# Performance work log

Measured on AMD Instinct MI355X. Metric: run time of the kernel, lower is better.

Reference implementation:

```python
import jax, jax.numpy as jnp
import numpy as np

NEG = -1.0e9
LN_EPS = 1e-5

B, S, M = 16, 1024, 256
H, L = 8, 2
DK = M // H  # 32


def setup_inputs() -> dict:
    key = jax.random.key(0)
    ks = jax.random.split(key, 10)
    adj = jax.random.randint(ks[0], (B, S, S), 0, 2).astype(jnp.int32)
    inputs = jax.random.normal(ks[1], (B, S, M), dtype=jnp.float32)
    score_mask = jax.random.randint(ks[2], (B, 1, S, S), 0, 2).astype(bool)
    # learned params: per layer H head projections Linear(M, DK), one attn Linear(2*DK, 1), LayerNorm(M)
    sc = 1.0 / np.sqrt(M)
    proj_w = jax.random.uniform(ks[3], (L, H, M, DK), jnp.float32, -sc, sc)
    proj_b = jax.random.uniform(ks[4], (L, H, DK), jnp.float32, -sc, sc)
    sa = 1.0 / np.sqrt(2 * DK)
    attn_w = jax.random.uniform(ks[5], (L, 2 * DK), jnp.float32, -sa, sa)
    attn_b = jax.random.uniform(ks[6], (L,), jnp.float32, -sa, sa)
    ln_g = jnp.ones((L, M), jnp.float32)
    ln_b = jnp.zeros((L, M), jnp.float32)
    return {"adj": adj, "inputs": inputs, "score_mask": score_mask, "type": 0,
            "proj_w": proj_w, "proj_b": proj_b, "attn_w": attn_w, "attn_b": attn_b,
            "ln_g": ln_g, "ln_b": ln_b}


def _layer(x, adj_l, smask, pw, pb, aw, ab, g, b):
    # x: [B,S,M]; per-head projection -> [B,H,S,DK]
    P = jnp.einsum('bsm,hmd->bhsd', x, pw) + pb[None, :, None, :]
    a1, a2 = aw[:DK], aw[DK:]
    # additive attention decomposed: score[b,h,i,j] = leaky_relu(a1.P_i + a2.P_j + ab)
    s1 = jnp.einsum('bhsd,d->bhs', P, a1)
    s2 = jnp.einsum('bhsd,d->bhs', P, a2)
    score = s1[..., :, None] + s2[..., None, :] + ab
    score = jnp.where(score >= 0, score, 0.2 * score)  # leaky_relu(0.2)
    score = jnp.where(smask, NEG, score)               # score_mask[:,0] broadcast over heads
    if adj_l is not None:
        score = jnp.where(adj_l[:, None] == 0, NEG, score)
    attn = jax.nn.softmax(score, axis=-1)
    out = jnp.einsum('bhij,bhjd->bhid', attn, P)       # [B,H,S,DK]
    concat = out.transpose(0, 2, 1, 3).reshape(x.shape[0], x.shape[1], -1)
    r = x + concat
    mu = jnp.mean(r, axis=-1, keepdims=True)
    var = jnp.mean((r - mu) ** 2, axis=-1, keepdims=True)
    return (r - mu) * jax.lax.rsqrt(var + LN_EPS) * g + b


def reference(adj, inputs, score_mask, type, proj_w, proj_b, attn_w, attn_b, ln_g, ln_b):
    # eval mode: DropBlock and both dropouts are identity
    semantic = (type == 1)
    smask = score_mask[:, 0][:, None]  # [B,1,S,S]
    x = inputs
    for l in range(L):
        adj_l = None if (semantic and l > 0) else adj
        x = _layer(x, adj_l, smask, proj_w[l], proj_b[l], attn_w[l], attn_b[l], ln_g[l], ln_b[l])
    return x
```

## Files before the change

### kernel.cpp

```cpp
#include <hip/hip_runtime.h>
#include <hip/hip_bf16.h>
#include <hip/hip_fp16.h>
#include <math.h>

#define NB 16
#define NS 1024
#define NM 256
#define NH 8
#define NDK 32
#define NL 2

typedef __attribute__((ext_vector_type(4))) float f32x4;
typedef __attribute__((ext_vector_type(8))) short bf16x8;
typedef __attribute__((ext_vector_type(4))) short bf16x4u;
typedef __attribute__((ext_vector_type(8))) _Float16 f16x8;
typedef __attribute__((ext_vector_type(2))) _Float16 f16x2;

#if __has_builtin(__builtin_amdgcn_exp2f)
#define EXP2F(x) __builtin_amdgcn_exp2f(x)
#else
#define EXP2F(x) exp2f(x)
#endif

__device__ __forceinline__ unsigned short f2h(float f) {
  _Float16 h = (_Float16)f;
  return __builtin_bit_cast(unsigned short, h);
}
__device__ __forceinline__ float h2f(unsigned short u) {
  return (float)__builtin_bit_cast(_Float16, u);
}

__device__ __forceinline__ unsigned int wword(unsigned int pw, unsigned int nw,
                                              f16x2 e1p2, f16x2 e1n2,
                                              unsigned int mk) {
  f16x2 hp = __builtin_bit_cast(f16x2, pw);
  f16x2 hn = __builtin_bit_cast(f16x2, nw);
  f16x2 w = __builtin_elementwise_max(hp * e1p2, hn * e1n2);
  return __builtin_bit_cast(unsigned int, w) & mk;
}

__global__ __launch_bounds__(256) void packbits_kernel(
    const int* __restrict__ src, unsigned int* __restrict__ dst, int inv)
{
  int wid = blockIdx.x * 4 + (threadIdx.x >> 6);
  int lane = threadIdx.x & 63;
  size_t eb = (size_t)wid * 2048;
  const int4* a4 = (const int4*)(src + eb);
  int lg = lane >> 3;
  int sh = (lane & 7) * 4;
  unsigned int xo = inv ? 15u : 0u;
#pragma unroll
  for (int k = 0; k < 8; ++k) {
    int4 v = a4[k * 64 + lane];
    unsigned int nc = ((v.x != 0) ? 1u : 0u) | ((v.y != 0) ? 2u : 0u) |
                      ((v.z != 0) ? 4u : 0u) | ((v.w != 0) ? 8u : 0u);
    nc ^= xo;
    unsigned int vc = nc << sh;
    vc |= __shfl_xor(vc, 1, 64);
    vc |= __shfl_xor(vc, 2, 64);
    vc |= __shfl_xor(vc, 4, 64);
    if ((lane & 7) == 0) dst[(size_t)wid * 64 + k * 8 + lg] = vc;
  }
}

__global__ __launch_bounds__(256) void maskcomb_kernel(
    unsigned int* __restrict__ pkc, const unsigned int* __restrict__ pks)
{
  int t = blockIdx.x * 256 + threadIdx.x;
  uint4 a = ((uint4*)pkc)[t];
  uint4 s = ((const uint4*)pks)[t];
  a.x |= s.x; a.y |= s.y; a.z |= s.z; a.w |= s.w;
  ((uint4*)pkc)[t] = a;
}

__global__ __launch_bounds__(256) void proj_kernel(
    const float* __restrict__ x,
    const float* __restrict__ pw,
    const float* __restrict__ pb,
    unsigned short* __restrict__ Pt)
{
  __shared__ unsigned short As[64][40];
  __shared__ unsigned short Bs[64][40];

  int ct = blockIdx.x;
  int rt = blockIdx.y;
  int t = threadIdx.x;
  int w = t >> 6, lane = t & 63;
  int il = lane & 15, g4 = lane >> 4;
  int wi = w >> 1, wc = w & 1;

  f32x4 acc[2][2] = {};

  int arow = t >> 2, akoff = (t & 3) * 8;
  int bcol = t & 63, bk0 = (t >> 6) * 8;
  int hd = ct * 64 + bcol;
  int h = hd >> 5, d = hd & 31;

  for (int k0 = 0; k0 < NM; k0 += 32) {
    const float* xp = x + (size_t)(rt * 64 + arow) * NM + k0 + akoff;
    f32x4 v0 = *(const f32x4*)xp;
    f32x4 v1 = *(const f32x4*)(xp + 4);
    unsigned short av[8];
    av[0] = f2h(v0[0]); av[1] = f2h(v0[1]); av[2] = f2h(v0[2]); av[3] = f2h(v0[3]);
    av[4] = f2h(v1[0]); av[5] = f2h(v1[1]); av[6] = f2h(v1[2]); av[7] = f2h(v1[3]);
    *(bf16x8*)&As[arow][akoff] = *(bf16x8*)av;
    const float* wp = pw + (size_t)h * NM * NDK + (size_t)(k0 + bk0) * NDK + d;
    unsigned short bv[8];
#pragma unroll
    for (int q = 0; q < 8; ++q) bv[q] = f2h(wp[q * NDK]);
    *(bf16x8*)&Bs[bcol][bk0] = *(bf16x8*)bv;
    __syncthreads();

    f16x8 af0 = *(f16x8*)&As[wi * 32 + il][g4 * 8];
    f16x8 af1 = *(f16x8*)&As[wi * 32 + 16 + il][g4 * 8];
    f16x8 bf0 = *(f16x8*)&Bs[wc * 32 + il][g4 * 8];
    f16x8 bf1 = *(f16x8*)&Bs[wc * 32 + 16 + il][g4 * 8];
    acc[0][0] = __builtin_amdgcn_mfma_f32_16x16x32_f16(af0, bf0, acc[0][0], 0, 0, 0);
    acc[0][1] = __builtin_amdgcn_mfma_f32_16x16x32_f16(af0, bf1, acc[0][1], 0, 0, 0);
    acc[1][0] = __builtin_amdgcn_mfma_f32_16x16x32_f16(af1, bf0, acc[1][0], 0, 0, 0);
    acc[1][1] = __builtin_amdgcn_mfma_f32_16x16x32_f16(af1, bf1, acc[1][1], 0, 0, 0);
    __syncthreads();
  }

#pragma unroll
  for (int ih = 0; ih < 2; ++ih) {
#pragma unroll
    for (int dh = 0; dh < 2; ++dh) {
      int colhd = ct * 64 + wc * 32 + dh * 16 + il;
      int hh = colhd >> 5, dd = colhd & 31;
      float bias = pb[colhd];
      int r0 = rt * 64 + wi * 32 + ih * 16 + g4 * 4;
      int bb = r0 >> 10, ss = r0 & 1023;
      f32x4 c = acc[ih][dh];
      unsigned short ov[4];
#pragma unroll
      for (int e = 0; e < 4; ++e) ov[e] = f2h(c[e] + bias);
      size_t idx = ((size_t)(bb * NH + hh) * NDK + dd) * NS + ss;
      *(bf16x4u*)(Pt + idx) = *(bf16x4u*)ov;
    }
  }
}

__global__ __launch_bounds__(256) void s_kernel(
    const unsigned short* __restrict__ Pt,
    const float* __restrict__ aw,
    const float* __restrict__ abp,
    float* __restrict__ s1o, unsigned short* __restrict__ s2po,
    unsigned short* __restrict__ s2no)
{
  const float LOG2E = 1.4426950408889634f;
  int t = blockIdx.x * 256 + threadIdx.x;
  int bh = t >> 10, s = t & 1023;
  const unsigned short* p = Pt + (size_t)bh * NDK * NS + s;
  float s1 = 0.f, s2 = 0.f;
#pragma unroll
  for (int dd = 0; dd < NDK; ++dd) {
    float pv = h2f(p[dd * NS]);
    s1 += pv * aw[dd];
    s2 += pv * aw[32 + dd];
  }
  float s2L = (s2 + abp[0]) * LOG2E;
  s2L = fminf(fmaxf(s2L, -7.5f), 7.5f);
  s1o[t] = s1 * LOG2E;
  s2po[t] = f2h(EXP2F(s2L));
  s2no[t] = f2h(EXP2F(0.2f * s2L));
}

__global__ __launch_bounds__(512) void attn_kernel(
    const unsigned short* __restrict__ Pt,
    const float* __restrict__ s1a,
    const unsigned short* __restrict__ s2pa,
    const unsigned short* __restrict__ s2na,
    const unsigned int* __restrict__ pkc,
    const unsigned int* __restrict__ pks,
    const int* __restrict__ typep,
    int layer,
    float* __restrict__ co)
{
  __shared__ __align__(16) unsigned short ptl[32 * 512];
  __shared__ __align__(16) unsigned short e2pl[1024];
  __shared__ __align__(16) unsigned short e2nl[1024];
  __shared__ uint4 mtab[256];

  int orig = blockIdx.x;
  int lb = (orig & 7) * 64 + (orig >> 3);
  int iq = lb & 3, bh = lb >> 2;
  int b = bh >> 3, h = bh & 7;

  int t = threadIdx.x, w = t >> 6, lane = t & 63;
  int il = lane & 15, g4 = lane >> 4;
  int xorv = (il & 7) << 4;

  if (t < 256) {
    unsigned int m = t;
    uint4 e;
    e.x = ((m & 1u)   ? 0u : 0xFFFFu) | ((m & 2u)   ? 0u : 0xFFFF0000u);
    e.y = ((m & 4u)   ? 0u : 0xFFFFu) | ((m & 8u)   ? 0u : 0xFFFF0000u);
    e.z = ((m & 16u)  ? 0u : 0xFFFFu) | ((m & 32u)  ? 0u : 0xFFFF0000u);
    e.w = ((m & 64u)  ? 0u : 0xFFFFu) | ((m & 128u) ? 0u : 0xFFFF0000u);
    mtab[t] = e;
  }

  const unsigned char* pkb =
      (const unsigned char*)((typep[0] == 1 && layer > 0) ? pks : pkc);
  const unsigned short* ptg = Pt + (size_t)bh * NDK * NS;

  f16x8 ones;
#pragma unroll
  for (int e = 0; e < 8; ++e) ones[e] = (_Float16)1.0f;

  int rbase = iq * 256 + w * 32;
  f16x2 e1p2[2], e1n2[2];
  const unsigned char* mrow[2];
#pragma unroll
  for (int g = 0; g < 2; ++g) {
    float s1L = s1a[(size_t)bh * NS + rbase + g * 16 + il];
    s1L = fminf(fmaxf(s1L, -7.5f), 7.5f);
    _Float16 hp = (_Float16)EXP2F(s1L);
    _Float16 hn = (_Float16)EXP2F(0.2f * s1L);
    e1p2[g][0] = hp; e1p2[g][1] = hp;
    e1n2[g][0] = hn; e1n2[g][1] = hn;
    mrow[g] = pkb + (((size_t)(b * NS + rbase + g * 16 + il) * NS) >> 3);
  }

  f32x4 acc[2][2] = {};
  f32x4 accd[2] = {};

  for (int jh = 0; jh < 2; ++jh) {
    __syncthreads();
    {
      const char* srcb = (const char*)ptg;
#pragma unroll
      for (int q = 0; q < 4; ++q) {
        int pos = q * 8192 + t * 16;
        int r = pos >> 10;
        int incol = pos & 1023;
        uint4 v = *(const uint4*)(srcb + r * 2048 + jh * 1024 + incol);
        *(uint4*)((char*)ptl + r * 1024 + (incol ^ ((r & 7) << 4))) = v;
      }
      if (jh == 0) {
        if (t < 128)
          ((uint4*)e2pl)[t] = *(const uint4*)(s2pa + (size_t)bh * NS + t * 8);
        else if (t < 256)
          ((uint4*)e2nl)[t - 128] =
              *(const uint4*)(s2na + (size_t)bh * NS + (t - 128) * 8);
      }
    }
    __syncthreads();

    for (int jg = 0; jg < 512; jg += 128) {
      uint4 mk0 = *(const uint4*)(mrow[0] + ((jh * 512 + jg) >> 3));
      uint4 mk1 = *(const uint4*)(mrow[1] + ((jh * 512 + jg) >> 3));
#pragma unroll
      for (int s = 0; s < 4; ++s) {
        unsigned int mb0 = ((&mk0.x)[s] >> (g4 * 8)) & 0xFFu;
        unsigned int mb1 = ((&mk1.x)[s] >> (g4 * 8)) & 0xFFu;
        uint4 am0 = mtab[mb0];
        uint4 am1 = mtab[mb1];
        int jl = jg + s * 32 + g4 * 8;
        int coff = (jl * 2) ^ xorv;
        const char* prow = (const char*)ptl + il * 1024;
        f16x8 b0 = *(const f16x8*)(prow + coff);
        f16x8 b1 = *(const f16x8*)(prow + 16 * 1024 + coff);
        int jfull = jh * 512 + jl;
        uint4 p4 = *(const uint4*)&e2pl[jfull];
        uint4 n4 = *(const uint4*)&e2nl[jfull];
        uint4 w0, w1;
        w0.x = wword(p4.x, n4.x, e1p2[0], e1n2[0], am0.x);
        w0.y = wword(p4.y, n4.y, e1p2[0], e1n2[0], am0.y);
        w0.z = wword(p4.z, n4.z, e1p2[0], e1n2[0], am0.z);
        w0.w = wword(p4.w, n4.w, e1p2[0], e1n2[0], am0.w);
        w1.x = wword(p4.x, n4.x, e1p2[1], e1n2[1], am1.x);
        w1.y = wword(p4.y, n4.y, e1p2[1], e1n2[1], am1.y);
        w1.z = wword(p4.z, n4.z, e1p2[1], e1n2[1], am1.z);
        w1.w = wword(p4.w, n4.w, e1p2[1], e1n2[1], am1.w);
        f16x8 af0 = __builtin_bit_cast(f16x8, w0);
        f16x8 af1 = __builtin_bit_cast(f16x8, w1);
        acc[0][0] = __builtin_amdgcn_mfma_f32_16x16x32_f16(af0, b0, acc[0][0], 0, 0, 0);
        acc[0][1] = __builtin_amdgcn_mfma_f32_16x16x32_f16(af0, b1, acc[0][1], 0, 0, 0);
        accd[0]   = __builtin_amdgcn_mfma_f32_16x16x32_f16(af0, ones, accd[0], 0, 0, 0);
        acc[1][0] = __builtin_amdgcn_mfma_f32_16x16x32_f16(af1, b0, acc[1][0], 0, 0, 0);
        acc[1][1] = __builtin_amdgcn_mfma_f32_16x16x32_f16(af1, b1, acc[1][1], 0, 0, 0);
        accd[1]   = __builtin_amdgcn_mfma_f32_16x16x32_f16(af1, ones, accd[1], 0, 0, 0);
      }
    }
  }

#pragma unroll
  for (int g = 0; g < 2; ++g) {
    f32x4 rd;
#pragma unroll
    for (int e = 0; e < 4; ++e) rd[e] = __builtin_amdgcn_rcpf(accd[g][e]);
    float* cob = co + (size_t)(b * NS + rbase + g * 16 + g4 * 4) * NM + h * 32 + il;
#pragma unroll
    for (int e = 0; e < 4; ++e) {
      cob[(size_t)e * NM] = acc[g][0][e] * rd[e];
      cob[(size_t)e * NM + 16] = acc[g][1][e] * rd[e];
    }
  }
}

__global__ __launch_bounds__(256) void ln_kernel(
    const float* __restrict__ xin, const float* __restrict__ co,
    const float* __restrict__ lng, const float* __restrict__ lnb,
    float* __restrict__ xout)
{
  int row = blockIdx.x * 4 + (threadIdx.x >> 6);
  int lane = threadIdx.x & 63;
  size_t base = (size_t)row * NM + lane * 4;
  f32x4 cv = *(const f32x4*)(co + base);
  f32x4 xv = *(const f32x4*)(xin + base);
  f32x4 r;
#pragma unroll
  for (int e = 0; e < 4; ++e) r[e] = cv[e] + xv[e];
  float sm = r[0] + r[1] + r[2] + r[3];
  float sq = r[0] * r[0] + r[1] * r[1] + r[2] * r[2] + r[3] * r[3];
#pragma unroll
  for (int off = 32; off >= 1; off >>= 1) {
    sm += __shfl_xor(sm, off, 64);
    sq += __shfl_xor(sq, off, 64);
  }
  float mu = sm * (1.f / 256.f);
  float var = sq * (1.f / 256.f) - mu * mu;
  float inv = rsqrtf(var + 1e-5f);
  f32x4 gv = *(const f32x4*)(lng + lane * 4);
  f32x4 bv = *(const f32x4*)(lnb + lane * 4);
  f32x4 o;
#pragma unroll
  for (int e = 0; e < 4; ++e) o[e] = (r[e] - mu) * inv * gv[e] + bv[e];
  *(f32x4*)(xout + base) = o;
}

extern "C" void kernel_launch(void* const* d_in, const int* in_sizes, int n_in,
                              void* d_out, int out_size, void* d_ws, size_t ws_size,
                              hipStream_t stream)
{
  const int* adj = (const int*)d_in[0];
  const float* inputs = (const float*)d_in[1];
  const int* smask = (const int*)d_in[2];
  const int* typep = (const int*)d_in[3];
  const float* proj_w = (const float*)d_in[4];
  const float* proj_b = (const float*)d_in[5];
  const float* attn_w = (const float*)d_in[6];
  const float* attn_b = (const float*)d_in[7];
  const float* ln_g = (const float*)d_in[8];
  const float* ln_b = (const float*)d_in[9];
  float* out = (float*)d_out;

  char* ws = (char*)d_ws;
  unsigned int* pkc = (unsigned int*)(ws);
  unsigned int* pks = (unsigned int*)(ws + (2u << 20));
  unsigned short* Pt = (unsigned short*)(ws + (4u << 20));
  float* s1 = (float*)(ws + (12u << 20));
  unsigned short* s2p = (unsigned short*)(ws + (12u << 20) + (1u << 19));
  unsigned short* s2n = (unsigned short*)(ws + (13u << 20));
  float* x1 = (float*)(ws + (14u << 20));
  float* co = out;

  packbits_kernel<<<2048, 256, 0, stream>>>(adj, pkc, 1);
  packbits_kernel<<<2048, 256, 0, stream>>>(smask, pks, 0);
  maskcomb_kernel<<<512, 256, 0, stream>>>(pkc, pks);

  for (int l = 0; l < NL; ++l) {
    const float* xin = (l == 0) ? inputs : x1;
    float* xout = (l == NL - 1) ? out : x1;
    proj_kernel<<<dim3(4, 256), 256, 0, stream>>>(
        xin, proj_w + (size_t)l * NH * NM * NDK, proj_b + (size_t)l * NH * NDK, Pt);
    s_kernel<<<512, 256, 0, stream>>>(Pt, attn_w + l * 64, attn_b + l, s1, s2p, s2n);
    attn_kernel<<<512, 512, 0, stream>>>(
        Pt, s1, s2p, s2n, pkc, pks, typep, l, co);
    ln_kernel<<<4096, 256, 0, stream>>>(xin, co, ln_g + l * NM, ln_b + l * NM, xout);
  }
}
```

Before: 128.0 us.

## Fuse score-vector computation into projection epilogue and pretranspose weights

Drops the separate s_kernel and computes s1/s2 inside the projection GEMM epilogue, using wave shuffles to reduce across the 16 lanes that hold one head's 32 dims. Adds a one-time wprep kernel that converts and transposes the projection weights to fp16 [h,d,m], so the GEMM B-tile loads become contiguous 16-byte reads instead of strided scalar float loads with conversion. Folds the mask-combine kernel into the second packbits pass through an OR into the adjacency bits. Together this cuts two launches per run plus the re-read of Pt, at the cost of an extra workspace buffer and s1/s2 now being computed from fp32 P values instead of fp16-rounded ones.

```diff
diff --git a/kernel.cpp b/kernel.cpp
--- a/kernel.cpp
+++ b/kernel.cpp
@@ -25,9 +25,6 @@
 __device__ __forceinline__ unsigned short f2h(float f) {
   _Float16 h = (_Float16)f;
   return __builtin_bit_cast(unsigned short, h);
-}
-__device__ __forceinline__ float h2f(unsigned short u) {
-  return (float)__builtin_bit_cast(_Float16, u);
 }
 
 __device__ __forceinline__ unsigned int wword(unsigned int pw, unsigned int nw,
@@ -40,7 +37,8 @@
 }
 
 __global__ __launch_bounds__(256) void packbits_kernel(
-    const int* __restrict__ src, unsigned int* __restrict__ dst, int inv)
+    const int* __restrict__ src, unsigned int* __restrict__ dst, int inv,
+    unsigned int* __restrict__ orc)
 {
   int wid = blockIdx.x * 4 + (threadIdx.x >> 6);
   int lane = threadIdx.x & 63;
@@ -59,29 +57,56 @@
     vc |= __shfl_xor(vc, 1, 64);
     vc |= __shfl_xor(vc, 2, 64);
     vc |= __shfl_xor(vc, 4, 64);
-    if ((lane & 7) == 0) dst[(size_t)wid * 64 + k * 8 + lg] = vc;
-  }
-}
-
-__global__ __launch_bounds__(256) void maskcomb_kernel(
-    unsigned int* __restrict__ pkc, const unsigned int* __restrict__ pks)
-{
-  int t = blockIdx.x * 256 + threadIdx.x;
-  uint4 a = ((uint4*)pkc)[t];
-  uint4 s = ((const uint4*)pks)[t];
-  a.x |= s.x; a.y |= s.y; a.z |= s.z; a.w |= s.w;
-  ((uint4*)pkc)[t] = a;
+    if ((lane & 7) == 0) {
+      size_t wi = (size_t)wid * 64 + k * 8 + lg;
+      dst[wi] = vc;
+      if (orc) orc[wi] |= vc;
+    }
+  }
+}
+
+__global__ __launch_bounds__(256) void wprep_kernel(
+    const float* __restrict__ pw, unsigned short* __restrict__ Wt)
+{
+  __shared__ float lw[256][36];
+  int lh = blockIdx.x;
+  int t = threadIdx.x;
+  const float* src = pw + (size_t)lh * NM * NDK;
+#pragma unroll
+  for (int q = 0; q < 8; ++q) {
+    int e0 = q * 1024 + t * 4;
+    int m = e0 >> 5, dc = e0 & 31;
+    f32x4 v = *(const f32x4*)(src + e0);
+    *(f32x4*)&lw[m][dc] = v;
+  }
+  __syncthreads();
+  unsigned short* out = Wt + (size_t)lh * NDK * NM;
+#pragma unroll
+  for (int q = 0; q < 4; ++q) {
+    int idx = q * 2048 + t * 8;
+    int d = idx >> 8, m = idx & 255;
+    unsigned short ov[8];
+#pragma unroll
+    for (int j = 0; j < 8; ++j) ov[j] = f2h(lw[m + j][d]);
+    *(uint4*)(out + (size_t)d * NM + m) = *(uint4*)ov;
+  }
 }
 
 __global__ __launch_bounds__(256) void proj_kernel(
     const float* __restrict__ x,
-    const float* __restrict__ pw,
+    const unsigned short* __restrict__ Wt,
     const float* __restrict__ pb,
-    unsigned short* __restrict__ Pt)
+    const float* __restrict__ aw,
+    const float* __restrict__ abp,
+    unsigned short* __restrict__ Pt,
+    float* __restrict__ s1o,
+    unsigned short* __restrict__ s2po,
+    unsigned short* __restrict__ s2no)
 {
   __shared__ unsigned short As[64][40];
   __shared__ unsigned short Bs[64][40];
 
+  const float LOG2E = 1.4426950408889634f;
   int ct = blockIdx.x;
   int rt = blockIdx.y;
   int t = threadIdx.x;
@@ -92,9 +117,7 @@
   f32x4 acc[2][2] = {};
 
   int arow = t >> 2, akoff = (t & 3) * 8;
-  int bcol = t & 63, bk0 = (t >> 6) * 8;
-  int hd = ct * 64 + bcol;
-  int h = hd >> 5, d = hd & 31;
+  int brow = t >> 2, bkoff = (t & 3) * 8;
 
   for (int k0 = 0; k0 < NM; k0 += 32) {
     const float* xp = x + (size_t)(rt * 64 + arow) * NM + k0 + akoff;
@@ -103,12 +126,9 @@
     unsigned short av[8];
     av[0] = f2h(v0[0]); av[1] = f2h(v0[1]); av[2] = f2h(v0[2]); av[3] = f2h(v0[3]);
     av[4] = f2h(v1[0]); av[5] = f2h(v1[1]); av[6] = f2h(v1[2]); av[7] = f2h(v1[3]);
-    *(bf16x8*)&As[arow][akoff] = *(bf16x8*)av;
-    const float* wp = pw + (size_t)h * NM * NDK + (size_t)(k0 + bk0) * NDK + d;
-    unsigned short bv[8];
-#pragma unroll
-    for (int q = 0; q < 8; ++q) bv[q] = f2h(wp[q * NDK]);
-    *(bf16x8*)&Bs[bcol][bk0] = *(bf16x8*)bv;
+    *(uint4*)&As[arow][akoff] = *(uint4*)av;
+    uint4 bv = *(const uint4*)(Wt + (size_t)(ct * 64 + brow) * NM + k0 + bkoff);
+    *(uint4*)&Bs[brow][bkoff] = bv;
     __syncthreads();
 
     f16x8 af0 = *(f16x8*)&As[wi * 32 + il][g4 * 8];
@@ -122,48 +142,54 @@
     __syncthreads();
   }
 
+  int head = ct * 2 + wc;
+  float a1v[2] = {aw[il], aw[16 + il]};
+  float a2v[2] = {aw[32 + il], aw[48 + il]};
+  float ab = abp[0];
+
 #pragma unroll
   for (int ih = 0; ih < 2; ++ih) {
+    float s1p[4] = {0.f, 0.f, 0.f, 0.f};
+    float s2p[4] = {0.f, 0.f, 0.f, 0.f};
+    int r0 = rt * 64 + wi * 32 + ih * 16 + g4 * 4;
+    int bb = r0 >> 10, ss = r0 & 1023;
 #pragma unroll
     for (int dh = 0; dh < 2; ++dh) {
       int colhd = ct * 64 + wc * 32 + dh * 16 + il;
-      int hh = colhd >> 5, dd = colhd & 31;
+      int dd = colhd & 31;
       float bias = pb[colhd];
-      int r0 = rt * 64 + wi * 32 + ih * 16 + g4 * 4;
-      int bb = r0 >> 10, ss = r0 & 1023;
       f32x4 c = acc[ih][dh];
       unsigned short ov[4];
 #pragma unroll
-      for (int e = 0; e < 4; ++e) ov[e] = f2h(c[e] + bias);
-      size_t idx = ((size_t)(bb * NH + hh) * NDK + dd) * NS + ss;
+      for (int e = 0; e < 4; ++e) {
+        float Pv = c[e] + bias;
+        ov[e] = f2h(Pv);
+        s1p[e] += Pv * a1v[dh];
+        s2p[e] += Pv * a2v[dh];
+      }
+      size_t idx = ((size_t)(bb * NH + head) * NDK + dd) * NS + ss;
       *(bf16x4u*)(Pt + idx) = *(bf16x4u*)ov;
     }
-  }
-}
-
-__global__ __launch_bounds__(256) void s_kernel(
-    const unsigned short* __restrict__ Pt,
-    const float* __restrict__ aw,
-    const float* __restrict__ abp,
-    float* __restrict__ s1o, unsigned short* __restrict__ s2po,
-    unsigned short* __restrict__ s2no)
-{
-  const float LOG2E = 1.4426950408889634f;
-  int t = blockIdx.x * 256 + threadIdx.x;
-  int bh = t >> 10, s = t & 1023;
-  const unsigned short* p = Pt + (size_t)bh * NDK * NS + s;
-  float s1 = 0.f, s2 = 0.f;
-#pragma unroll
-  for (int dd = 0; dd < NDK; ++dd) {
-    float pv = h2f(p[dd * NS]);
-    s1 += pv * aw[dd];
-    s2 += pv * aw[32 + dd];
-  }
-  float s2L = (s2 + abp[0]) * LOG2E;
-  s2L = fminf(fmaxf(s2L, -7.5f), 7.5f);
-  s1o[t] = s1 * LOG2E;
-  s2po[t] = f2h(EXP2F(s2L));
-  s2no[t] = f2h(EXP2F(0.2f * s2L));
+#pragma unroll
+    for (int e = 0; e < 4; ++e) {
+#pragma unroll
+      for (int off = 1; off <= 8; off <<= 1) {
+        s1p[e] += __shfl_xor(s1p[e], off, 64);
+        s2p[e] += __shfl_xor(s2p[e], off, 64);
+      }
+    }
+    if (il == 0) {
+      size_t sb = (size_t)(bb * NH + head) * NS + ss;
+#pragma unroll
+      for (int e = 0; e < 4; ++e) {
+        s1o[sb + e] = s1p[e] * LOG2E;
+        float s2L = (s2p[e] + ab) * LOG2E;
+        s2L = fminf(fmaxf(s2L, -7.5f), 7.5f);
+        s2po[sb + e] = f2h(EXP2F(s2L));
+        s2no[sb + e] = f2h(EXP2F(0.2f * s2L));
+      }
+    }
+  }
 }
 
 __global__ __launch_bounds__(512) void attn_kernel(
@@ -355,18 +381,19 @@
   unsigned short* s2p = (unsigned short*)(ws + (12u << 20) + (1u << 19));
   unsigned short* s2n = (unsigned short*)(ws + (13u << 20));
   float* x1 = (float*)(ws + (14u << 20));
+  unsigned short* Wt = (unsigned short*)(ws + (30u << 20));
   float* co = out;
 
-  packbits_kernel<<<2048, 256, 0, stream>>>(adj, pkc, 1);
-  packbits_kernel<<<2048, 256, 0, stream>>>(smask, pks, 0);
-  maskcomb_kernel<<<512, 256, 0, stream>>>(pkc, pks);
+  packbits_kernel<<<2048, 256, 0, stream>>>(adj, pkc, 1, nullptr);
+  packbits_kernel<<<2048, 256, 0, stream>>>(smask, pks, 0, pkc);
+  wprep_kernel<<<16, 256, 0, stream>>>(proj_w, Wt);
 
   for (int l = 0; l < NL; ++l) {
     const float* xin = (l == 0) ? inputs : x1;
     float* xout = (l == NL - 1) ? out : x1;
     proj_kernel<<<dim3(4, 256), 256, 0, stream>>>(
-        xin, proj_w + (size_t)l * NH * NM * NDK, proj_b + (size_t)l * NH * NDK, Pt);
-    s_kernel<<<512, 256, 0, stream>>>(Pt, attn_w + l * 64, attn_b + l, s1, s2p, s2n);
+        xin, Wt + (size_t)l * NH * NDK * NM, proj_b + (size_t)l * NH * NDK,
+        attn_w + l * 64, attn_b + l, Pt, s1, s2p, s2n);
     attn_kernel<<<512, 512, 0, stream>>>(
         Pt, s1, s2p, s2n, pkc, pks, typep, l, co);
     ln_kernel<<<4096, 256, 0, stream>>>(xin, co, ln_g + l * NM, ln_b + l * NM, xout);
```

Result: no change. 128.0 us (-0.0%).
